# Optimization experiments

Hardware: AMD Instinct MI355X
Metric: run time of the kernel (lower is better)

Reference implementation:

```python
import jax, jax.numpy as jnp
import numpy as np
import math

NUM_HEADS = 16
NUM_KV_HEADS = 4
HEAD_DIM = 128
ROPE_THETA = 10000.0


def _rope(x, cos, sin):
    # x: [b, h, s, d]; cos/sin: [1, 1, s, d//2]
    half = x.shape[-1] // 2
    x1, x2 = x[..., :half], x[..., half:]
    return jnp.concatenate([x1 * cos - x2 * sin, x2 * cos + x1 * sin], axis=-1)


def setup_inputs() -> dict:
    key = jax.random.key(0)
    ks = jax.random.split(key, 5)
    B, S, H = 2, 2048, 2048
    scale_qk = (2.0 / (H + H)) ** 0.5
    scale_kv = (2.0 / (H + NUM_KV_HEADS * HEAD_DIM)) ** 0.5
    return {
        "hidden_states": jax.random.normal(ks[0], (B, S, H), jnp.float32),
        "Wq": jax.random.normal(ks[1], (NUM_HEADS * HEAD_DIM, H), jnp.float32) * scale_qk,
        "Wk": jax.random.normal(ks[2], (NUM_KV_HEADS * HEAD_DIM, H), jnp.float32) * scale_kv,
        "Wv": jax.random.normal(ks[3], (NUM_KV_HEADS * HEAD_DIM, H), jnp.float32) * scale_kv,
        "Wo": jax.random.normal(ks[4], (NUM_HEADS * HEAD_DIM, H), jnp.float32) * scale_qk,
    }


def reference(hidden_states, Wq, Wk, Wv, Wo):
    B, S, H = hidden_states.shape
    hd = HEAD_DIM

    q = (hidden_states @ Wq.T).reshape(B, S, NUM_HEADS, hd).transpose(0, 2, 1, 3)
    k = (hidden_states @ Wk.T).reshape(B, S, NUM_KV_HEADS, hd).transpose(0, 2, 1, 3)
    v = (hidden_states @ Wv.T).reshape(B, S, NUM_KV_HEADS, hd).transpose(0, 2, 1, 3)

    # RoPE (half-split variant, as in module)
    inv_freq = 1.0 / (ROPE_THETA ** (jnp.arange(0, hd, 2, dtype=jnp.float32) / hd))
    pos = jnp.arange(S, dtype=jnp.float32)
    freqs = pos[:, None] * inv_freq[None, :]           # [S, hd//2]
    cos = jnp.cos(freqs)[None, None]                   # [1,1,S,hd//2]
    sin = jnp.sin(freqs)[None, None]
    q = _rope(q, cos, sin)
    k = _rope(k, cos, sin)

    # GQA: repeat kv heads (repeat_interleave semantics)
    n_rep = NUM_HEADS // NUM_KV_HEADS
    k = jnp.repeat(k, n_rep, axis=1)
    v = jnp.repeat(v, n_rep, axis=1)

    scores = jnp.einsum("bhqd,bhkd->bhqk", q, k) / math.sqrt(hd)
    attn = jax.nn.softmax(scores, axis=-1)
    out = jnp.einsum("bhqk,bhkd->bhqd", attn, v)
    out = out.transpose(0, 2, 1, 3).reshape(B, S, NUM_HEADS * hd)
    return out @ Wo.T
```

## Files before the change

kernel.cpp:

```cpp
#include <hip/hip_runtime.h>
#include <cstdint>
#include <cstddef>

typedef __bf16 bf16x8 __attribute__((ext_vector_type(8)));
typedef __bf16 bf16x4 __attribute__((ext_vector_type(4)));
typedef float  f32x4  __attribute__((ext_vector_type(4)));

__device__ __forceinline__ void gload_lds16(const void* g, void* l) {
    __builtin_amdgcn_global_load_lds(
        (const __attribute__((address_space(1))) void*)g,
        (__attribute__((address_space(3))) void*)l, 16, 0, 0);
}

#define WAITB4 asm volatile("s_waitcnt vmcnt(4) lgkmcnt(0)\ns_barrier" ::: "memory")
#define WAITB0 asm volatile("s_waitcnt vmcnt(0) lgkmcnt(0)\ns_barrier" ::: "memory")

#define SEQ 2048
#define NH 16
#define NKV 4
#define HD 128

__global__ __launch_bounds__(256) void cvt_all(const float* __restrict__ hs,
                                               const float* __restrict__ wq,
                                               const float* __restrict__ wk,
                                               const float* __restrict__ wv,
                                               const float* __restrict__ wo,
                                               __bf16* __restrict__ hB,
                                               __bf16* __restrict__ WqkB,
                                               __bf16* __restrict__ WvB,
                                               __bf16* __restrict__ WoB) {
    int bid = blockIdx.x;
    const float* in; __bf16* out; int base;
    if (bid < 8192)        { in = hs; out = hB;                   base = bid; }
    else if (bid < 12288)  { in = wq; out = WqkB;                 base = bid - 8192; }
    else if (bid < 13312)  { in = wk; out = WqkB + 2048 * 2048;   base = bid - 12288; }
    else if (bid < 14336)  { in = wv; out = WvB;                  base = bid - 13312; }
    else                   { in = wo; out = WoB;                  base = bid - 14336; }
    int i = base * 256 + threadIdx.x;
    float4 v = ((const float4*)in)[i];
    bf16x4 o = { (__bf16)v.x, (__bf16)v.y, (__bf16)v.z, (__bf16)v.w };
    ((bf16x4*)out)[i] = o;
}

__device__ __forceinline__ void stage256(const __bf16* __restrict__ Amat,
                                         const __bf16* __restrict__ Bmat,
                                         char* ldsbuf, int bm, int bn, int k0,
                                         int wave, int lane) {
#pragma unroll
    for (int tt = 0; tt < 2; ++tt) {
        int c = wave * 2 + tt;
        int row = ((c & 3) << 6) + lane;
        int ko = (c >> 2) << 3;
        gload_lds16(Amat + (size_t)(bm + row) * 2048 + k0 + ko, ldsbuf + c * 1024);
        gload_lds16(Bmat + (size_t)(bn + row) * 2048 + k0 + ko, ldsbuf + 16384 + c * 1024);
    }
}

__device__ __forceinline__ void mfma_tile256(const char* buf, int quad, int l16,
                                             int wr128, int colbase,
                                             f32x4 acc[8][4]) {
    const __bf16* bA = (const __bf16*)buf;
    const __bf16* bB = bA + 8192;
    bf16x8 af[8], bq[4];
#pragma unroll
    for (int i = 0; i < 8; ++i)
        af[i] = *(const bf16x8*)(bA + quad * 2048 + (wr128 + i * 16 + l16) * 8);
#pragma unroll
    for (int j = 0; j < 4; ++j)
        bq[j] = *(const bf16x8*)(bB + quad * 2048 +
                                 (colbase + (j & 1) * 16 + (j >> 1) * 64 + l16) * 8);
    __builtin_amdgcn_s_setprio(1);
#pragma unroll
    for (int i = 0; i < 8; ++i)
#pragma unroll
        for (int j = 0; j < 4; ++j)
            acc[i][j] = __builtin_amdgcn_mfma_f32_16x16x32_bf16(
                af[i], bq[j], acc[i][j], 0, 0, 0);
    __builtin_amdgcn_s_setprio(0);
}

__global__ __launch_bounds__(512, 2) void qkv_gemm(const __bf16* __restrict__ hB,
                                                   const __bf16* __restrict__ Wqk,
                                                   const __bf16* __restrict__ Wv,
                                                   __bf16* __restrict__ Qr,
                                                   __bf16* __restrict__ Kr,
                                                   __bf16* __restrict__ VT) {
    __shared__ __align__(16) char lds[3 * 32768];
    const int tid = threadIdx.x;
    const int wave = tid >> 6, lane = tid & 63;
    const int quad = lane >> 4, l16 = lane & 15;
    const int wr = wave >> 2, wc = wave & 3;
    const int x = blockIdx.x, y = blockIdx.y;
    const bool isVT = (y >= 10);
    const bool isQ = (y < 8);

    const __bf16* Amat = isVT ? Wv : hB;
    const __bf16* Bmat = isVT ? hB : (isQ ? Wqk : Wqk + 2048 * 2048);
    const int bm = isVT ? (y - 10) * 256 : x * 256;
    const int bn = isVT ? x * 256 : (isQ ? y * 256 : (y - 8) * 256);

    const int wr128 = wr * 128;
    const int colbase = (wc >> 1) * 128 + (wc & 1) * 32;

    f32x4 acc[8][4] = {};

    stage256(Amat, Bmat, lds, bm, bn, 0, wave, lane);
    stage256(Amat, Bmat, lds + 32768, bm, bn, 32, wave, lane);

    int cb = 0;
    for (int t = 0; t < 63; ++t) {
        WAITB4;
        if (t < 62) {
            int sb = cb + 2; if (sb >= 3) sb -= 3;
            stage256(Amat, Bmat, lds + sb * 32768, bm, bn, (t + 2) * 32, wave, lane);
        }
        mfma_tile256(lds + cb * 32768, quad, l16, wr128, colbase, acc);
        if (++cb == 3) cb = 0;
    }
    WAITB0;
    mfma_tile256(lds + cb * 32768, quad, l16, wr128, colbase, acc);

    if (isVT) {
#pragma unroll
        for (int i = 0; i < 8; ++i)
#pragma unroll
            for (int j = 0; j < 4; ++j) {
                int row = bm + wr128 + i * 16 + quad * 4;
                int col = bn + colbase + (j & 1) * 16 + (j >> 1) * 64 + l16;
#pragma unroll
                for (int r = 0; r < 4; ++r)
                    VT[(size_t)(row + r) * 4096 + col] = (__bf16)acc[i][j][r];
            }
    } else {
        __bf16* outp = isQ ? Qr : Kr;
        const float sc = isQ ? 0.08838834764831845f : 1.0f;
        const int nh = isQ ? NH : NKV;
        const int hh = (isQ ? y * 2 : (y - 8) * 2) + (wc >> 1);
#pragma unroll
        for (int j2 = 0; j2 < 2; ++j2) {
            int d = (wc & 1) * 32 + j2 * 16 + l16;
            float inv = exp2f(-(float)d * 0.2076205059304601f);
#pragma unroll
            for (int i = 0; i < 8; ++i)
#pragma unroll
                for (int r = 0; r < 4; ++r) {
                    int m = bm + wr128 + i * 16 + quad * 4 + r;
                    int s = m & (SEQ - 1), b = m >> 11;
                    float f = (float)s * inv;
                    float c = __cosf(f) * sc, sn = __sinf(f) * sc;
                    float x1 = acc[i][j2][r], x2 = acc[i][j2 + 2][r];
                    size_t rb = ((size_t)(b * nh + hh) * SEQ + s) * HD;
                    outp[rb + d]      = (__bf16)(x1 * c - x2 * sn);
                    outp[rb + d + 64] = (__bf16)(x2 * c + x1 * sn);
                }
        }
    }
}

__global__ __launch_bounds__(512, 2) void gemm_bt_f32(const __bf16* __restrict__ A,
                                                      const __bf16* __restrict__ W,
                                                      float* __restrict__ C) {
    __shared__ __align__(16) char lds[3 * 32768];
    const int tid = threadIdx.x;
    const int wave = tid >> 6, lane = tid & 63;
    const int quad = lane >> 4, l16 = lane & 15;
    const int wr = wave >> 2, wc = wave & 3;
    const int bm = blockIdx.x * 256, bn = blockIdx.y * 256;
    const int wr128 = wr * 128;
    const int colbase = (wc >> 1) * 128 + (wc & 1) * 32;

    f32x4 acc[8][4] = {};

    stage256(A, W, lds, bm, bn, 0, wave, lane);
    stage256(A, W, lds + 32768, bm, bn, 32, wave, lane);

    int cb = 0;
    for (int t = 0; t < 63; ++t) {
        WAITB4;
        if (t < 62) {
            int sb = cb + 2; if (sb >= 3) sb -= 3;
            stage256(A, W, lds + sb * 32768, bm, bn, (t + 2) * 32, wave, lane);
        }
        mfma_tile256(lds + cb * 32768, quad, l16, wr128, colbase, acc);
        if (++cb == 3) cb = 0;
    }
    WAITB0;
    mfma_tile256(lds + cb * 32768, quad, l16, wr128, colbase, acc);

#pragma unroll
    for (int i = 0; i < 8; ++i)
#pragma unroll
        for (int j = 0; j < 4; ++j) {
            int row = bm + wr128 + i * 16 + quad * 4;
            int col = bn + colbase + (j & 1) * 16 + (j >> 1) * 64 + l16;
#pragma unroll
            for (int r = 0; r < 4; ++r)
                C[(size_t)(row + r) * 2048 + col] = acc[i][j][r];
        }
}

__global__ __launch_bounds__(512, 1) void attn_kernel(const __bf16* __restrict__ Q,
                                                      const __bf16* __restrict__ Kr,
                                                      const __bf16* __restrict__ VT,
                                                      __bf16* __restrict__ AO) {
    __shared__ __align__(16) char ring[3 * 32768];
    __shared__ __align__(16) __bf16 Pb[8][32][72];

    const int tid = threadIdx.x;
    const int wave = tid >> 6, lane = tid & 63;
    const int quad = lane >> 4, l16 = lane & 15;
    const int h = blockIdx.y, b = blockIdx.z;
    const int kv = h >> 2;
    const int qbase = blockIdx.x * 256 + wave * 32;

    bf16x8 qf[2][4];
#pragma unroll
    for (int qs = 0; qs < 2; ++qs) {
        const __bf16* Qp =
            Q + ((size_t)(b * NH + h) * SEQ + qbase + qs * 16 + l16) * HD + quad * 8;
#pragma unroll
        for (int kq = 0; kq < 4; ++kq) qf[qs][kq] = *(const bf16x8*)(Qp + kq * 32);
    }

    const __bf16* Kp = Kr + (size_t)(b * NKV + kv) * SEQ * HD;
    const __bf16* Vp = VT + (size_t)(kv * HD) * (2 * SEQ) + b * SEQ;

    f32x4 oacc[2][8] = {};
    float lpart[2] = {0.f, 0.f};

    auto stage = [&](int sb, int k0) {
        char* dst = ring + sb * 32768;
#pragma unroll
        for (int tt = 0; tt < 4; ++tt) {
            int c = wave * 4 + tt;
            if (c < 16) {
                gload_lds16(Kp + (size_t)(k0 + lane) * HD + c * 8, dst + c * 1024);
            } else {
                int vc = c - 16;
                gload_lds16(Vp + (size_t)(((vc & 1) << 6) + lane) * (2 * SEQ) + k0 +
                                (vc >> 1) * 8,
                            dst + c * 1024);
            }
        }
    };

    auto compute = [&](int cb) {
        const __bf16* kt = (const __bf16*)(ring + cb * 32768);
        const __bf16* vt = kt + 8192;
#pragma unroll
        for (int mt = 0; mt < 4; ++mt) {
            f32x4 s0 = {0.f, 0.f, 0.f, 0.f}, s1 = {0.f, 0.f, 0.f, 0.f};
#pragma unroll
            for (int kq = 0; kq < 4; ++kq) {
                bf16x8 ka = *(const bf16x8*)(kt + (kq * 4 + quad) * 512 +
                                             (mt * 16 + l16) * 8);
                s0 = __builtin_amdgcn_mfma_f32_16x16x32_bf16(ka, qf[0][kq], s0, 0, 0, 0);
                s1 = __builtin_amdgcn_mfma_f32_16x16x32_bf16(ka, qf[1][kq], s1, 0, 0, 0);
            }
            bf16x4 pk0, pk1;
#pragma unroll
            for (int r = 0; r < 4; ++r) {
                float p0 = __expf(s0[r]);
                float p1 = __expf(s1[r]);
                lpart[0] += p0; lpart[1] += p1;
                pk0[r] = (__bf16)p0; pk1[r] = (__bf16)p1;
            }
            *(bf16x4*)&Pb[wave][l16][mt * 16 + quad * 4] = pk0;
            *(bf16x4*)&Pb[wave][16 + l16][mt * 16 + quad * 4] = pk1;
        }
#pragma unroll
        for (int kk = 0; kk < 2; ++kk) {
            bf16x8 pb0 = *(const bf16x8*)&Pb[wave][l16][kk * 32 + quad * 8];
            bf16x8 pb1 = *(const bf16x8*)&Pb[wave][16 + l16][kk * 32 + quad * 8];
#pragma unroll
            for (int mt = 0; mt < 8; ++mt) {
                bf16x8 va = *(const bf16x8*)(vt + (kk * 4 + quad) * 1024 +
                                             (mt * 16 + l16) * 8);
                oacc[0][mt] = __builtin_amdgcn_mfma_f32_16x16x32_bf16(
                    va, pb0, oacc[0][mt], 0, 0, 0);
                oacc[1][mt] = __builtin_amdgcn_mfma_f32_16x16x32_bf16(
                    va, pb1, oacc[1][mt], 0, 0, 0);
            }
        }
    };

    stage(0, 0);
    stage(1, 64);

    int cb = 0;
    for (int t = 0; t < 31; ++t) {
        WAITB4;
        if (t < 30) {
            int sb = cb + 2; if (sb >= 3) sb -= 3;
            stage(sb, (t + 2) * 64);
        }
        compute(cb);
        if (++cb == 3) cb = 0;
    }
    WAITB0;
    compute(cb);

#pragma unroll
    for (int qs = 0; qs < 2; ++qs) {
        lpart[qs] += __shfl_xor(lpart[qs], 16);
        lpart[qs] += __shfl_xor(lpart[qs], 32);
        float inv = 1.f / lpart[qs];
        int q = qbase + qs * 16 + l16;
#pragma unroll
        for (int mt = 0; mt < 8; ++mt) {
            bf16x4 ov;
#pragma unroll
            for (int r = 0; r < 4; ++r) ov[r] = (__bf16)(oacc[qs][mt][r] * inv);
            *(bf16x4*)(AO + ((size_t)(b * SEQ + q)) * (NH * HD) + h * HD +
                       mt * 16 + quad * 4) = ov;
        }
    }
}

extern "C" void kernel_launch(void* const* d_in, const int* in_sizes, int n_in,
                              void* d_out, int out_size, void* d_ws, size_t ws_size,
                              hipStream_t stream) {
    const float* hs = (const float*)d_in[0];
    const float* Wq = (const float*)d_in[1];
    const float* Wk = (const float*)d_in[2];
    const float* Wv = (const float*)d_in[3];
    const float* Wo = (const float*)d_in[4];
    float* out = (float*)d_out;
    char* ws = (char*)d_ws;

    __bf16* Qr   = (__bf16*)(ws + 0);
    __bf16* Kr   = (__bf16*)(ws + 16777216);
    __bf16* VT   = (__bf16*)(ws + 20971520);
    __bf16* WoB  = (__bf16*)(ws + 25165824);
    __bf16* hB   = (__bf16*)(ws + 33554432);
    __bf16* WqkB = (__bf16*)(ws + 50331648);
    __bf16* WvB  = (__bf16*)(ws + 60817408);
    __bf16* AO   = (__bf16*)(ws + 33554432);

    cvt_all<<<18432, 256, 0, stream>>>(hs, Wq, Wk, Wv, Wo, hB, WqkB, WvB, WoB);

    qkv_gemm<<<dim3(16, 12), 512, 0, stream>>>(hB, WqkB, WvB, Qr, Kr, VT);

    attn_kernel<<<dim3(8, 16, 2), 512, 0, stream>>>(Qr, Kr, VT, AO);

    gemm_bt_f32<<<dim3(16, 8), 512, 0, stream>>>(AO, WoB, out);
}
```

Baseline: 365.0 us.

## Rework GEMM mainloop into double-buffered K=64 with interleaved half-tile prefetch

```diff
diff --git a/kernel.cpp b/kernel.cpp
--- a/kernel.cpp
+++ b/kernel.cpp
@@ -12,6 +12,10 @@
         (__attribute__((address_space(3))) void*)l, 16, 0, 0);
 }
 
+#define VM6B asm volatile("s_waitcnt vmcnt(6) lgkmcnt(0)\ns_barrier" ::: "memory")
+#define VM4B asm volatile("s_waitcnt vmcnt(4) lgkmcnt(0)\ns_barrier" ::: "memory")
+#define VM0B asm volatile("s_waitcnt vmcnt(0) lgkmcnt(0)\ns_barrier" ::: "memory")
+#define BARO asm volatile("s_barrier" ::: "memory")
 #define WAITB4 asm volatile("s_waitcnt vmcnt(4) lgkmcnt(0)\ns_barrier" ::: "memory")
 #define WAITB0 asm volatile("s_waitcnt vmcnt(0) lgkmcnt(0)\ns_barrier" ::: "memory")
 
@@ -42,41 +46,87 @@
     ((bf16x4*)out)[i] = o;
 }
 
-__device__ __forceinline__ void stage256(const __bf16* __restrict__ Amat,
-                                         const __bf16* __restrict__ Bmat,
-                                         char* ldsbuf, int bm, int bn, int k0,
-                                         int wave, int lane) {
-#pragma unroll
-    for (int tt = 0; tt < 2; ++tt) {
-        int c = wave * 2 + tt;
-        int row = ((c & 3) << 6) + lane;
-        int ko = (c >> 2) << 3;
-        gload_lds16(Amat + (size_t)(bm + row) * 2048 + k0 + ko, ldsbuf + c * 1024);
-        gload_lds16(Bmat + (size_t)(bn + row) * 2048 + k0 + ko, ldsbuf + 16384 + c * 1024);
-    }
-}
-
-__device__ __forceinline__ void mfma_tile256(const char* buf, int quad, int l16,
-                                             int wr128, int colbase,
-                                             f32x4 acc[8][4]) {
-    const __bf16* bA = (const __bf16*)buf;
-    const __bf16* bB = bA + 8192;
-    bf16x8 af[8], bq[4];
-#pragma unroll
-    for (int i = 0; i < 8; ++i)
-        af[i] = *(const bf16x8*)(bA + quad * 2048 + (wr128 + i * 16 + l16) * 8);
-#pragma unroll
-    for (int j = 0; j < 4; ++j)
-        bq[j] = *(const bf16x8*)(bB + quad * 2048 +
-                                 (colbase + (j & 1) * 16 + (j >> 1) * 64 + l16) * 8);
+__device__ __forceinline__ void stage_half(const __bf16* __restrict__ M,
+                                           char* dbuf, int bmn, int k0, int half,
+                                           int wave, int lane) {
+    char* hb = dbuf + (half & 1) * 32768 + (half >> 1) * 16384;
+    int kbase = k0 + (half >> 1) * 32;
+#pragma unroll
+    for (int g = 0; g < 2; ++g) {
+        int c = wave * 2 + g;
+        int row = (c & 3) * 64 + lane;
+        int ks = c >> 2;
+        gload_lds16(M + (size_t)(bmn + row) * 2048 + kbase + ks * 8, hb + c * 1024);
+    }
+}
+
+template <int KS, int MH>
+__device__ __forceinline__ void phase_mfma(const __bf16* bA, const __bf16* bB,
+                                           int quad, int l16, int wr128, int colbase,
+                                           bf16x8 (&bq)[4], f32x4 acc[8][4]) {
+    bf16x8 af[4];
+#pragma unroll
+    for (int ii = 0; ii < 4; ++ii)
+        af[ii] = *(const bf16x8*)(bA + (KS * 4 + quad) * 2048 +
+                                  (wr128 + (MH * 4 + ii) * 16 + l16) * 8);
+    if (MH == 0) {
+#pragma unroll
+        for (int j = 0; j < 4; ++j)
+            bq[j] = *(const bf16x8*)(bB + (KS * 4 + quad) * 2048 +
+                                     (colbase + (j & 1) * 16 + (j >> 1) * 64 + l16) * 8);
+    }
     __builtin_amdgcn_s_setprio(1);
 #pragma unroll
-    for (int i = 0; i < 8; ++i)
+    for (int ii = 0; ii < 4; ++ii)
 #pragma unroll
         for (int j = 0; j < 4; ++j)
-            acc[i][j] = __builtin_amdgcn_mfma_f32_16x16x32_bf16(
-                af[i], bq[j], acc[i][j], 0, 0, 0);
+            acc[MH * 4 + ii][j] = __builtin_amdgcn_mfma_f32_16x16x32_bf16(
+                af[ii], bq[j], acc[MH * 4 + ii][j], 0, 0, 0);
     __builtin_amdgcn_s_setprio(0);
+}
+
+__device__ __forceinline__ void gemm_core(const __bf16* __restrict__ A,
+                                          const __bf16* __restrict__ B,
+                                          char* lds, int bm, int bn,
+                                          int wave, int lane, int quad, int l16,
+                                          int wr128, int colbase, f32x4 acc[8][4]) {
+    const int NT = 32;
+    stage_half(A, lds, bm, 0, 0, wave, lane);
+    stage_half(B, lds, bn, 0, 1, wave, lane);
+    stage_half(A, lds, bm, 0, 2, wave, lane);
+    stage_half(B, lds, bn, 0, 3, wave, lane);
+    int cur = 0;
+    for (int t = 0; t < NT - 1; ++t) {
+        const __bf16* bA = (const __bf16*)(lds + cur * 65536);
+        const __bf16* bB = (const __bf16*)(lds + cur * 65536 + 32768);
+        char* nb = lds + (cur ^ 1) * 65536;
+        int k1 = (t + 1) * 64;
+        bf16x8 bq[4];
+        stage_half(A, nb, bm, k1, 0, wave, lane);
+        VM6B;
+        phase_mfma<0, 0>(bA, bB, quad, l16, wr128, colbase, bq, acc);
+        stage_half(B, nb, bn, k1, 1, wave, lane);
+        BARO;
+        phase_mfma<0, 1>(bA, bB, quad, l16, wr128, colbase, bq, acc);
+        stage_half(A, nb, bm, k1, 2, wave, lane);
+        VM6B;
+        phase_mfma<1, 0>(bA, bB, quad, l16, wr128, colbase, bq, acc);
+        stage_half(B, nb, bn, k1, 3, wave, lane);
+        BARO;
+        phase_mfma<1, 1>(bA, bB, quad, l16, wr128, colbase, bq, acc);
+        cur ^= 1;
+    }
+    {
+        const __bf16* bA = (const __bf16*)(lds + cur * 65536);
+        const __bf16* bB = (const __bf16*)(lds + cur * 65536 + 32768);
+        bf16x8 bq[4];
+        VM4B;
+        phase_mfma<0, 0>(bA, bB, quad, l16, wr128, colbase, bq, acc);
+        phase_mfma<0, 1>(bA, bB, quad, l16, wr128, colbase, bq, acc);
+        VM0B;
+        phase_mfma<1, 0>(bA, bB, quad, l16, wr128, colbase, bq, acc);
+        phase_mfma<1, 1>(bA, bB, quad, l16, wr128, colbase, bq, acc);
+    }
 }
 
 __global__ __launch_bounds__(512, 2) void qkv_gemm(const __bf16* __restrict__ hB,
@@ -85,7 +135,7 @@
                                                    __bf16* __restrict__ Qr,
                                                    __bf16* __restrict__ Kr,
                                                    __bf16* __restrict__ VT) {
-    __shared__ __align__(16) char lds[3 * 32768];
+    __shared__ __align__(16) char lds[2 * 65536];
     const int tid = threadIdx.x;
     const int wave = tid >> 6, lane = tid & 63;
     const int quad = lane >> 4, l16 = lane & 15;
@@ -103,22 +153,7 @@
     const int colbase = (wc >> 1) * 128 + (wc & 1) * 32;
 
     f32x4 acc[8][4] = {};
-
-    stage256(Amat, Bmat, lds, bm, bn, 0, wave, lane);
-    stage256(Amat, Bmat, lds + 32768, bm, bn, 32, wave, lane);
-
-    int cb = 0;
-    for (int t = 0; t < 63; ++t) {
-        WAITB4;
-        if (t < 62) {
-            int sb = cb + 2; if (sb >= 3) sb -= 3;
-            stage256(Amat, Bmat, lds + sb * 32768, bm, bn, (t + 2) * 32, wave, lane);
-        }
-        mfma_tile256(lds + cb * 32768, quad, l16, wr128, colbase, acc);
-        if (++cb == 3) cb = 0;
-    }
-    WAITB0;
-    mfma_tile256(lds + cb * 32768, quad, l16, wr128, colbase, acc);
+    gemm_core(Amat, Bmat, lds, bm, bn, wave, lane, quad, l16, wr128, colbase, acc);
 
     if (isVT) {
 #pragma unroll
@@ -160,7 +195,7 @@
 __global__ __launch_bounds__(512, 2) void gemm_bt_f32(const __bf16* __restrict__ A,
                                                       const __bf16* __restrict__ W,
                                                       float* __restrict__ C) {
-    __shared__ __align__(16) char lds[3 * 32768];
+    __shared__ __align__(16) char lds[2 * 65536];
     const int tid = threadIdx.x;
     const int wave = tid >> 6, lane = tid & 63;
     const int quad = lane >> 4, l16 = lane & 15;
@@ -170,22 +205,7 @@
     const int colbase = (wc >> 1) * 128 + (wc & 1) * 32;
 
     f32x4 acc[8][4] = {};
-
-    stage256(A, W, lds, bm, bn, 0, wave, lane);
-    stage256(A, W, lds + 32768, bm, bn, 32, wave, lane);
-
-    int cb = 0;
-    for (int t = 0; t < 63; ++t) {
-        WAITB4;
-        if (t < 62) {
-            int sb = cb + 2; if (sb >= 3) sb -= 3;
-            stage256(A, W, lds + sb * 32768, bm, bn, (t + 2) * 32, wave, lane);
-        }
-        mfma_tile256(lds + cb * 32768, quad, l16, wr128, colbase, acc);
-        if (++cb == 3) cb = 0;
-    }
-    WAITB0;
-    mfma_tile256(lds + cb * 32768, quad, l16, wr128, colbase, acc);
+    gemm_core(A, W, lds, bm, bn, wave, lane, quad, l16, wr128, colbase, acc);
 
 #pragma unroll
     for (int i = 0; i < 8; ++i)
```

Result: no change. 361.7 us (-0.9%).
